# Kernel optimization log

Measured on AMD Instinct MI355X. Metric: run time of the kernel, lower is better.

Reference implementation:

```python
import jax, jax.numpy as jnp
import numpy as np

B, T, D = 64, 2048, 256  # batch, seq_len, embedding_dim; units == embedding_dim == D
U = 256


def setup_inputs() -> dict:
    key = jax.random.key(0)
    ks = jax.random.split(key, 8)
    s = 1.0 / np.sqrt(D)
    return {
        "features": jax.random.normal(ks[0], (B, T, D), dtype=jnp.float32),
        "hidden": jax.random.normal(ks[1], (B, D), dtype=jnp.float32),
        "w1_w": jax.random.uniform(ks[2], (U, D), jnp.float32, -s, s),
        "w1_b": jax.random.uniform(ks[3], (U,), jnp.float32, -s, s),
        "w2_w": jax.random.uniform(ks[4], (U, D), jnp.float32, -s, s),
        "w2_b": jax.random.uniform(ks[5], (U,), jnp.float32, -s, s),
        "v_w": jax.random.uniform(ks[6], (1, U), jnp.float32, -s, s),
        "v_b": jax.random.uniform(ks[7], (1,), jnp.float32, -s, s),
    }


def reference(features, hidden, w1_w, w1_b, w2_w, w2_b, v_w, v_b):
    # features: [B, T, D], hidden: [B, D]
    proj = jnp.einsum('btd,ud->btu', features, w1_w) + w1_b  # w1(features)
    hid = jnp.einsum('bd,ud->bu', hidden, w2_w) + w2_b        # w2(hidden)
    score = jnp.einsum('btu,ou->bto', jnp.tanh(proj + hid[:, None, :]), v_w) + v_b  # [B,T,1]
    attn = jax.nn.softmax(score, axis=1)                      # [B,T,1]
    context = jnp.sum(attn * features, axis=1)                # [B,D]
    return context, attn
```

## Files before the change

### kernel.cpp

```cpp
#include <hip/hip_runtime.h>
#include <stdint.h>

#define Bq 64
#define Tq 2048
#define Dq 256
#define Uq 256
#define NTILE 32

typedef __bf16 bf16x8 __attribute__((ext_vector_type(8)));
typedef float f32x4 __attribute__((ext_vector_type(4)));

#define ASTR 1040
#define ABUF (4 * ASTR)
#define BSTR 4128
#define BBUF (4 * BSTR)

__device__ inline unsigned short rne_bf16(float a) {
  unsigned b = __float_as_uint(a);
  return (unsigned short)((b + 0x7FFFu + ((b >> 16) & 1u)) >> 16);
}

__device__ inline float fast_tanh(float x) {
  float e = __expf(2.0f * x);
  return 1.0f - 2.0f * __builtin_amdgcn_rcpf(e + 1.0f);
}

__global__ void k01_prep(const float* __restrict__ w1,
                         unsigned short* __restrict__ w1bf,
                         const float* __restrict__ hidden,
                         const float* __restrict__ w2_w,
                         const float* __restrict__ w2_b,
                         const float* __restrict__ w1_b,
                         float* __restrict__ comb) {
  if (blockIdx.x < 64) {
    int idx = blockIdx.x * 256 + threadIdx.x;
    int i = idx * 4;
    int u = i >> 8;
    int k = i & 255;
    float4 v = *reinterpret_cast<const float4*>(&w1[i]);
    ushort4 h;
    h.x = rne_bf16(v.x);
    h.y = rne_bf16(v.y);
    h.z = rne_bf16(v.z);
    h.w = rne_bf16(v.w);
    int dst = (k >> 3) * (Uq * 8) + u * 8 + (k & 7);
    *reinterpret_cast<ushort4*>(&w1bf[dst]) = h;
  } else {
    int bid = blockIdx.x - 64;
    int b = bid >> 6;
    int wave = threadIdx.x >> 6;
    int lane = threadIdx.x & 63;
    int u = (bid & 63) * 4 + wave;
    const float* h = hidden + b * Dq;
    const float* w = w2_w + u * Dq;
    float sum = 0.f;
#pragma unroll
    for (int i = 0; i < Dq; i += 64) sum += h[lane + i] * w[lane + i];
#pragma unroll
    for (int m = 32; m >= 1; m >>= 1) sum += __shfl_xor(sum, m, 64);
    if (lane == 0) comb[b * Uq + u] = sum + w2_b[u] + w1_b[u];
  }
}

__global__ __launch_bounds__(256) void k2_score(
    const float* __restrict__ feat, const unsigned short* __restrict__ w1bf,
    const float* __restrict__ comb, const float* __restrict__ v_w,
    const float* __restrict__ v_b, float* __restrict__ score,
    float* __restrict__ pm, float* __restrict__ partc) {
  __shared__ char sB[2 * BBUF];
  __shared__ char sA[2 * ABUF];
  __shared__ float scp[4 * 64];
  __shared__ float ebuf[64];
  const int b = blockIdx.y;
  const int tile = blockIdx.x;
  const int t0 = tile * 64;
  const int tid = threadIdx.x;
  const int w = tid >> 6;
  const int l = tid & 63;
  const int fr = l & 15;
  const int g = l >> 4;

  const int arow = tid >> 2;
  const int aoct = tid & 3;
  const float* aload = feat + ((size_t)(b * Tq + t0 + arow)) * Dq + aoct * 8;
  char* const awr = sA + aoct * ASTR + arow * 16;

  f32x4 acc[4][4] = {};
  float4 pa[2][2];

  auto issueBdma = [&](int c) {
    char* bbase = sB + (c & 1) * BBUF;
#pragma unroll
    for (int q = 0; q < 4; ++q) {
      int d = w * 4 + q;
      int j = d >> 2;
      int h2 = d & 3;
      const unsigned short* src =
          w1bf + (size_t)(c * 4 + j) * (Uq * 8) + (h2 * 64 + l) * 8;
      __builtin_amdgcn_global_load_lds(
          (const __attribute__((address_space(1))) unsigned int*)src,
          (__attribute__((address_space(3))) unsigned int*)(bbase + j * BSTR +
                                                            h2 * 1024),
          16, 0, 0);
    }
  };
  auto loadA = [&](int c) {
    pa[c & 1][0] = *reinterpret_cast<const float4*>(aload + c * 32);
    pa[c & 1][1] = *reinterpret_cast<const float4*>(aload + c * 32 + 4);
  };
  auto writeA = [&](int c) {
    const float4& v0 = pa[c & 1][0];
    const float4& v1 = pa[c & 1][1];
    uint4 H;
    H.x = rne_bf16(v0.x) | ((unsigned)rne_bf16(v0.y) << 16);
    H.y = rne_bf16(v0.z) | ((unsigned)rne_bf16(v0.w) << 16);
    H.z = rne_bf16(v1.x) | ((unsigned)rne_bf16(v1.y) << 16);
    H.w = rne_bf16(v1.z) | ((unsigned)rne_bf16(v1.w) << 16);
    *reinterpret_cast<uint4*>(awr + (c & 1) * ABUF) = H;
  };
  auto pipeBarrier = [&]() {
    __builtin_amdgcn_sched_barrier(0);
    asm volatile("s_waitcnt vmcnt(2) lgkmcnt(0)" ::: "memory");
    __builtin_amdgcn_s_barrier();
    __builtin_amdgcn_sched_barrier(0);
  };

  issueBdma(0);
  __builtin_amdgcn_sched_barrier(0);
  loadA(0);
  loadA(1);
  __builtin_amdgcn_sched_barrier(0);
  writeA(0);
  pipeBarrier();

#pragma unroll
  for (int c = 0; c < 8; ++c) {
    if (c < 7) {
      issueBdma(c + 1);
      __builtin_amdgcn_sched_barrier(0);
      loadA((c + 2) & 7);
      __builtin_amdgcn_sched_barrier(0);
    }
    const char* bA = sA + (c & 1) * ABUF;
    const char* bB = sB + (c & 1) * BBUF;
    bf16x8 ah[4], bh[4];
#pragma unroll
    for (int mf = 0; mf < 4; ++mf)
      ah[mf] = *reinterpret_cast<const bf16x8*>(bA + g * ASTR +
                                                (mf * 16 + fr) * 16);
#pragma unroll
    for (int nf = 0; nf < 4; ++nf)
      bh[nf] = *reinterpret_cast<const bf16x8*>(
          bB + g * BSTR + (w * 64 + nf * 16 + fr) * 16);
    __builtin_amdgcn_s_setprio(1);
#pragma unroll
    for (int mf = 0; mf < 4; ++mf)
#pragma unroll
      for (int nf = 0; nf < 4; ++nf)
        acc[mf][nf] = __builtin_amdgcn_mfma_f32_16x16x32_bf16(
            ah[mf], bh[nf], acc[mf][nf], 0, 0, 0);
    __builtin_amdgcn_s_setprio(0);
    if (c < 7) {
      writeA(c + 1);
      pipeBarrier();
    }
  }

  float cb[4], vw4[4];
#pragma unroll
  for (int nf = 0; nf < 4; ++nf) {
    int u = w * 64 + nf * 16 + fr;
    cb[nf] = comb[b * Uq + u];
    vw4[nf] = v_w[u];
  }
  float sc[4][4];
#pragma unroll
  for (int mf = 0; mf < 4; ++mf)
#pragma unroll
    for (int r = 0; r < 4; ++r) sc[mf][r] = 0.f;
#pragma unroll
  for (int mf = 0; mf < 4; ++mf)
#pragma unroll
    for (int nf = 0; nf < 4; ++nf)
#pragma unroll
      for (int r = 0; r < 4; ++r)
        sc[mf][r] += vw4[nf] * fast_tanh(acc[mf][nf][r] + cb[nf]);
#pragma unroll
  for (int m = 1; m < 16; m <<= 1)
#pragma unroll
    for (int mf = 0; mf < 4; ++mf)
#pragma unroll
      for (int r = 0; r < 4; ++r) sc[mf][r] += __shfl_xor(sc[mf][r], m, 16);
  __syncthreads();
  if (fr == 0) {
#pragma unroll
    for (int mf = 0; mf < 4; ++mf)
#pragma unroll
      for (int r = 0; r < 4; ++r)
        scp[w * 64 + mf * 16 + g * 4 + r] = sc[mf][r];
  }
  __syncthreads();
  if (tid < 64) {
    float v =
        scp[tid] + scp[64 + tid] + scp[128 + tid] + scp[192 + tid] + v_b[0];
    score[b * Tq + t0 + tid] = v;
    float m = v;
#pragma unroll
    for (int mk = 32; mk >= 1; mk >>= 1) m = fmaxf(m, __shfl_xor(m, mk, 64));
    ebuf[tid] = __expf(v - m);
    if (tid == 0) pm[b * NTILE + tile] = m;
  }
  __syncthreads();
  {
    const float* frow = feat + (size_t)(b * Tq + t0) * Dq + tid;
    float cd = 0.f;
#pragma unroll 8
    for (int t = 0; t < 64; ++t) cd += ebuf[t] * frow[(size_t)t * Dq];
    partc[((size_t)b * NTILE + tile) * Dq + tid] = cd;
  }
}

__global__ void k3_softmax(float* __restrict__ s, float* __restrict__ stats) {
  int b = blockIdx.x;
  int tid = threadIdx.x;
  const int base = b * Tq;
  float v[8];
  float m = -1e30f;
#pragma unroll
  for (int i = 0; i < 8; ++i) {
    v[i] = s[base + tid + 256 * i];
    m = fmaxf(m, v[i]);
  }
#pragma unroll
  for (int mk = 32; mk >= 1; mk >>= 1) m = fmaxf(m, __shfl_xor(m, mk, 64));
  __shared__ float red[4];
  int wv = tid >> 6, ln = tid & 63;
  if (ln == 0) red[wv] = m;
  __syncthreads();
  m = fmaxf(fmaxf(red[0], red[1]), fmaxf(red[2], red[3]));
  __syncthreads();
  float sum = 0.f;
#pragma unroll
  for (int i = 0; i < 8; ++i) {
    v[i] = __expf(v[i] - m);
    sum += v[i];
  }
#pragma unroll
  for (int mk = 32; mk >= 1; mk >>= 1) sum += __shfl_xor(sum, mk, 64);
  if (ln == 0) red[wv] = sum;
  __syncthreads();
  sum = red[0] + red[1] + red[2] + red[3];
  float inv = 1.f / sum;
#pragma unroll
  for (int i = 0; i < 8; ++i) s[base + tid + 256 * i] = v[i] * inv;
  if (tid == 0) {
    stats[b * 2 + 0] = m;
    stats[b * 2 + 1] = inv;
  }
}

__global__ void k5_combine(const float* __restrict__ partc,
                           const float* __restrict__ pm,
                           const float* __restrict__ stats,
                           float* __restrict__ ctx) {
  int b = blockIdx.x;
  int d = threadIdx.x;
  const float M = stats[b * 2 + 0];
  const float invS = stats[b * 2 + 1];
  __shared__ float wgt[NTILE];
  if (d < NTILE) wgt[d] = __expf(pm[b * NTILE + d] - M);
  __syncthreads();
  float s = 0.f;
#pragma unroll
  for (int j = 0; j < NTILE; ++j)
    s += wgt[j] * partc[((size_t)b * NTILE + j) * Dq + d];
  ctx[b * Dq + d] = s * invS;
}

extern "C" void kernel_launch(void* const* d_in, const int* in_sizes, int n_in,
                              void* d_out, int out_size, void* d_ws,
                              size_t ws_size, hipStream_t stream) {
  const float* feat   = (const float*)d_in[0];
  const float* hidden = (const float*)d_in[1];
  const float* w1_w   = (const float*)d_in[2];
  const float* w1_b   = (const float*)d_in[3];
  const float* w2_w   = (const float*)d_in[4];
  const float* w2_b   = (const float*)d_in[5];
  const float* v_w    = (const float*)d_in[6];
  const float* v_b    = (const float*)d_in[7];

  float* ctx  = (float*)d_out;
  float* attn = ctx + Bq * Dq;
  float* comb = (float*)d_ws;
  unsigned short* w1bf = (unsigned short*)(comb + Bq * Uq);
  float* partc = (float*)(w1bf + Uq * Dq);
  float* pm    = partc + (size_t)Bq * NTILE * Dq;
  float* stats = pm + Bq * NTILE;

  k01_prep<<<64 + Bq * 64, 256, 0, stream>>>(w1_w, w1bf, hidden, w2_w, w2_b,
                                             w1_b, comb);
  k2_score<<<dim3(NTILE, Bq), 256, 0, stream>>>(feat, w1bf, comb, v_w, v_b,
                                                attn, pm, partc);
  k3_softmax<<<Bq, 256, 0, stream>>>(attn, stats);
  k5_combine<<<Bq, 256, 0, stream>>>(partc, pm, stats, ctx);
}
```

Before: 68.84 us.

## Prefetch feature rows into registers early and fuse softmax with combine kernel

In the score kernel, the feature rows needed for the partial context sum are now loaded into registers before the score epilogue and its barriers, with the remaining rows loaded in staggered chunks, so their memory latency overlaps other work. Separately, the softmax and the final combine kernels are merged into one, which removes a launch and the stats round-trip through global memory. The prefetch adds 64 live float registers per thread and could lower occupancy in the MFMA kernel.

```diff
diff --git a/kernel.cpp b/kernel.cpp
--- a/kernel.cpp
+++ b/kernel.cpp
@@ -166,6 +166,13 @@
     }
   }
 
+  const float* frow = feat + (size_t)(b * Tq + t0) * Dq + tid;
+  float fv0[16], fv1[16];
+#pragma unroll
+  for (int t = 0; t < 16; ++t) fv0[t] = frow[(size_t)t * Dq];
+#pragma unroll
+  for (int t = 0; t < 16; ++t) fv1[t] = frow[(size_t)(t + 16) * Dq];
+
   float cb[4], vw4[4];
 #pragma unroll
   for (int nf = 0; nf < 4; ++nf) {
@@ -212,15 +219,28 @@
   }
   __syncthreads();
   {
-    const float* frow = feat + (size_t)(b * Tq + t0) * Dq + tid;
+    float fv2[16], fv3[16];
+#pragma unroll
+    for (int t = 0; t < 16; ++t) fv2[t] = frow[(size_t)(t + 32) * Dq];
     float cd = 0.f;
-#pragma unroll 8
-    for (int t = 0; t < 64; ++t) cd += ebuf[t] * frow[(size_t)t * Dq];
+#pragma unroll
+    for (int t = 0; t < 16; ++t) cd += ebuf[t] * fv0[t];
+#pragma unroll
+    for (int t = 0; t < 16; ++t) fv3[t] = frow[(size_t)(t + 48) * Dq];
+#pragma unroll
+    for (int t = 0; t < 16; ++t) cd += ebuf[t + 16] * fv1[t];
+#pragma unroll
+    for (int t = 0; t < 16; ++t) cd += ebuf[t + 32] * fv2[t];
+#pragma unroll
+    for (int t = 0; t < 16; ++t) cd += ebuf[t + 48] * fv3[t];
     partc[((size_t)b * NTILE + tile) * Dq + tid] = cd;
   }
 }
 
-__global__ void k3_softmax(float* __restrict__ s, float* __restrict__ stats) {
+__global__ void k35_softmax_combine(float* __restrict__ s,
+                                    const float* __restrict__ pm,
+                                    const float* __restrict__ partc,
+                                    float* __restrict__ ctx) {
   int b = blockIdx.x;
   int tid = threadIdx.x;
   const int base = b * Tq;
@@ -253,28 +273,15 @@
   float inv = 1.f / sum;
 #pragma unroll
   for (int i = 0; i < 8; ++i) s[base + tid + 256 * i] = v[i] * inv;
-  if (tid == 0) {
-    stats[b * 2 + 0] = m;
-    stats[b * 2 + 1] = inv;
-  }
-}
-
-__global__ void k5_combine(const float* __restrict__ partc,
-                           const float* __restrict__ pm,
-                           const float* __restrict__ stats,
-                           float* __restrict__ ctx) {
-  int b = blockIdx.x;
-  int d = threadIdx.x;
-  const float M = stats[b * 2 + 0];
-  const float invS = stats[b * 2 + 1];
+
   __shared__ float wgt[NTILE];
-  if (d < NTILE) wgt[d] = __expf(pm[b * NTILE + d] - M);
-  __syncthreads();
-  float s = 0.f;
+  if (tid < NTILE) wgt[tid] = __expf(pm[b * NTILE + tid] - m);
+  __syncthreads();
+  float cs = 0.f;
 #pragma unroll
   for (int j = 0; j < NTILE; ++j)
-    s += wgt[j] * partc[((size_t)b * NTILE + j) * Dq + d];
-  ctx[b * Dq + d] = s * invS;
+    cs += wgt[j] * partc[((size_t)b * NTILE + j) * Dq + tid];
+  ctx[b * Dq + tid] = cs * inv;
 }
 
 extern "C" void kernel_launch(void* const* d_in, const int* in_sizes, int n_in,
@@ -295,12 +302,10 @@
   unsigned short* w1bf = (unsigned short*)(comb + Bq * Uq);
   float* partc = (float*)(w1bf + Uq * Dq);
   float* pm    = partc + (size_t)Bq * NTILE * Dq;
-  float* stats = pm + Bq * NTILE;
 
   k01_prep<<<64 + Bq * 64, 256, 0, stream>>>(w1_w, w1bf, hidden, w2_w, w2_b,
                                              w1_b, comb);
   k2_score<<<dim3(NTILE, Bq), 256, 0, stream>>>(feat, w1bf, comb, v_w, v_b,
                                                 attn, pm, partc);
-  k3_softmax<<<Bq, 256, 0, stream>>>(attn, stats);
-  k5_combine<<<Bq, 256, 0, stream>>>(partc, pm, stats, ctx);
-}
+  k35_softmax_combine<<<Bq, 256, 0, stream>>>(attn, pm, partc, ctx);
+}
```

Measured after the change: 62.10 us. 1.11x faster.
